# Optimization experiments

Hardware: AMD Instinct MI355X
Metric: run time of the kernel (lower is better)

The kernel has to match this reference:

```python
import jax, jax.numpy as jnp
import numpy as np

S = 1024   # query_len == key_len (self-attention)
B = 4      # batch
E = 1024   # embed_dim
H = 16     # num_heads
D = E // H # head_dim = 64
PE = 2 * S # positional table rows


def setup_inputs() -> dict:
    rng = jax.random.key(0)
    ks = jax.random.split(rng, 12)
    f = lambda k, sh, s: jax.random.normal(k, sh, dtype=jnp.float32) * s
    W = 0.02  # weight scale (xavier-ish for E=1024)
    return {
        'query': f(ks[0], (S, B, E), 1.0),
        'key': f(ks[1], (S, B, E), 1.0),
        'value': f(ks[2], (S, B, E), 1.0),
        'pe': f(ks[3], (PE, E), 1.0),
        'w_q': f(ks[4], (E, E), W),
        'w_k': f(ks[5], (E, E), W),
        'w_v': f(ks[6], (E, E), W),
        'w_k_pos': f(ks[7], (E, E), W),
        'content_bias': f(ks[8], (H, D), 0.02),
        'pos_bias': f(ks[9], (H, D), 0.02),
        'w_out': f(ks[10], (E, E), W),
        'b_out': f(ks[11], (E,), 0.02),
    }


def _rel_shift(pos):
    # pos: [B, H, Q, M] with M = 2*K - 1. Transformer-XL pad/narrow shift trick.
    Bn, h, Q, M = pos.shape
    p = jnp.pad(pos, ((0, 0), (0, 0), (0, 1), (0, 1)))          # [B,H,Q+1,M+1]
    p = p.reshape(Bn, h, (Q + 1) * (M + 1))
    p = p[:, :, M // 2: M // 2 + M * Q].reshape(Bn, h, Q, M)
    return p[..., :(M + 1) // 2]                                 # [B,H,Q,K]


def reference(query, key, value, pe, w_q, w_k, w_v, w_k_pos,
              content_bias, pos_bias, w_out, b_out):
    Q, Bn, Em = query.shape
    K = key.shape[0]
    h, d = content_bias.shape
    scaling = d ** -0.5

    # projections (nn.Linear: x @ W.T), split heads -> [B,H,len,d]
    q = (query @ w_q.T).reshape(Q, Bn, h, d).transpose(1, 2, 0, 3)
    k = (key   @ w_k.T).reshape(K, Bn, h, d).transpose(1, 2, 0, 3)
    v = (value @ w_v.T).reshape(K, Bn, h, d).transpose(1, 2, 0, 3)

    # relative position keys: centered slice of pe table, size 2K-1
    M = 2 * K - 1
    lower = pe.shape[0] // 2 - K + 1  # offset = 0
    k_pos = (pe[lower:lower + M] @ w_k_pos.T).reshape(M, h, d).transpose(1, 0, 2)  # [H,M,d]

    content = jnp.einsum('bhqd,bhkd->bhqk', q + content_bias[None, :, None, :], k)
    pos = jnp.einsum('bhqd,hmd->bhqm', q + pos_bias[None, :, None, :], k_pos)
    pos = _rel_shift(pos)  # [B,H,Q,K]

    attn = jax.nn.softmax((content + pos) * scaling, axis=-1)
    out = jnp.einsum('bhqk,bhkd->bhqd', attn, v)        # [B,H,Q,d]
    out = out.transpose(2, 0, 1, 3).reshape(Q, Bn, Em)  # [Q,B,E]
    return out @ w_out.T + b_out
```

## Files before the change

### kernel.cpp

```cpp
#include <hip/hip_runtime.h>


typedef short s16x8 __attribute__((ext_vector_type(8)));
typedef __bf16 bf16x8 __attribute__((ext_vector_type(8)));
typedef float f32x4 __attribute__((ext_vector_type(4)));
typedef unsigned int u32;

__device__ __forceinline__ float b2f(short s) {
  u32 u = ((u32)(unsigned short)s) << 16;
  return __builtin_bit_cast(float, u);
}
__device__ __forceinline__ short f2b(float f) {
  u32 u = __builtin_bit_cast(u32, f);
  u32 r = u + 0x7FFFu + ((u >> 16) & 1u);
  return (short)(r >> 16);
}

__device__ __forceinline__ f32x4 mfma_bf16(s16x8 a, s16x8 b, f32x4 c) {
  return __builtin_amdgcn_mfma_f32_16x16x32_bf16(
      __builtin_bit_cast(bf16x8, a), __builtin_bit_cast(bf16x8, b), c, 0, 0, 0);
}

__device__ __forceinline__ void glds16(void* l, const void* g) {
  __builtin_amdgcn_global_load_lds(
      (const __attribute__((address_space(1))) void*)g,
      (__attribute__((address_space(3))) void*)l, 16, 0, 0);
}

__device__ __forceinline__ int swz(int row, int unit) {
  return row * 128 + ((unit ^ (row & 7)) << 4);
}

__global__ __launch_bounds__(256) void cvt_all(
    const float* __restrict__ q, const float* __restrict__ k,
    const float* __restrict__ v, const float* __restrict__ pe,
    const float* __restrict__ wq, const float* __restrict__ wk,
    const float* __restrict__ wv, const float* __restrict__ wkp,
    const float* __restrict__ wo, short* __restrict__ dst)
{
  const int c = blockIdx.x * 256 + threadIdx.x;
  int idx = c * 8;
  const float* src;
  if      (idx < 4194304)  { src = q; }
  else if (idx < 8388608)  { src = k;   idx -= 4194304; }
  else if (idx < 12582912) { src = v;   idx -= 8388608; }
  else if (idx < 14680064) { src = pe;  idx -= 12582912; }
  else if (idx < 15728640) { src = wq;  idx -= 14680064; }
  else if (idx < 16777216) { src = wk;  idx -= 15728640; }
  else if (idx < 17825792) { src = wv;  idx -= 16777216; }
  else if (idx < 18874368) { src = wkp; idx -= 17825792; }
  else                     { src = wo;  idx -= 18874368; }
  float4 x = *(const float4*)(src + idx);
  float4 y = *(const float4*)(src + idx + 4);
  s16x8 o;
  o[0] = f2b(x.x); o[1] = f2b(x.y); o[2] = f2b(x.z); o[3] = f2b(x.w);
  o[4] = f2b(y.x); o[5] = f2b(y.y); o[6] = f2b(y.z); o[7] = f2b(y.w);
  *(s16x8*)(dst + (long)c * 8) = o;
}

__device__ __forceinline__ void gemm_core_bf16(
    const short* __restrict__ A, const short* __restrict__ W,
    short* At, short* Wt, f32x4 (&acc)[4][4], int bm, int bn)
{
  const int t = threadIdx.x;
  const int lane = t & 63, w = t >> 6;
  const int wm = w >> 1, wn = w & 1;
  const int quad = lane >> 4, lo16 = lane & 15;
  const int srow = t >> 2;
  const int skc = (t & 3) * 8;
  const int soff = t * 16;

  const short* Ag0 = A + (bm * 128 + srow) * 1024 + skc;
  const short* Wg0 = W + (bn * 128 + srow) * 1024 + skc;
  char* AtB = (char*)At;
  char* WtB = (char*)Wt;

  for (int k0 = 0; k0 < 1024; k0 += 32) {
    glds16(AtB + soff,        Ag0 + k0);
    glds16(AtB + 4096 + soff, Ag0 + 64 * 1024 + k0);
    glds16(WtB + soff,        Wg0 + k0);
    glds16(WtB + 4096 + soff, Wg0 + 64 * 1024 + k0);
    __syncthreads();
    s16x8 af[4], bfr[4];
#pragma unroll
    for (int mt = 0; mt < 4; ++mt)
      af[mt] = *(const s16x8*)(At + (wm * 64 + mt * 16 + lo16) * 32 + quad * 8);
#pragma unroll
    for (int nt = 0; nt < 4; ++nt)
      bfr[nt] = *(const s16x8*)(Wt + (wn * 64 + nt * 16 + lo16) * 32 + quad * 8);
#pragma unroll
    for (int mt = 0; mt < 4; ++mt)
#pragma unroll
      for (int nt = 0; nt < 4; ++nt)
        acc[mt][nt] = mfma_bf16(af[mt], bfr[nt], acc[mt][nt]);
    __syncthreads();
  }
}

__global__ __launch_bounds__(256) void proj_gemm(
    const short* __restrict__ qsrc, const short* __restrict__ ksrc,
    const short* __restrict__ vsrc, const short* __restrict__ pesrc,
    const short* __restrict__ wqb, const short* __restrict__ wkb,
    const short* __restrict__ wvb, const short* __restrict__ wkpb,
    short* __restrict__ qo, short* __restrict__ ko,
    short* __restrict__ vo, short* __restrict__ po)
{
  const int z = blockIdx.z;
  const short* A; const short* W; int M;
  if (z == 0)      { A = qsrc;  W = wqb;  M = 4096; }
  else if (z == 1) { A = ksrc;  W = wkb;  M = 4096; }
  else if (z == 2) { A = vsrc;  W = wvb;  M = 4096; }
  else             { A = pesrc; W = wkpb; M = 2048; }
  const int bm = blockIdx.x, bn = blockIdx.y;
  if (bm * 128 >= M) return;

  __shared__ __align__(16) short At[128 * 32];
  __shared__ __align__(16) short Wt[128 * 32];
  f32x4 acc[4][4] = {};
  gemm_core_bf16(A, W, At, Wt, acc, bm, bn);

  const int t = threadIdx.x;
  const int lane = t & 63, w = t >> 6;
  const int wm = w >> 1, wn = w & 1;
  const int quad = lane >> 4, lo16 = lane & 15;
#pragma unroll
  for (int mt = 0; mt < 4; ++mt) {
#pragma unroll
    for (int nt = 0; nt < 4; ++nt) {
#pragma unroll
      for (int r = 0; r < 4; ++r) {
        int m = bm * 128 + wm * 64 + mt * 16 + quad * 4 + r;
        int n = bn * 128 + wn * 64 + nt * 16 + lo16;
        short val = f2b(acc[mt][nt][r]);
        if (z <= 1) {
          short* o = (z == 0) ? qo : ko;
          int s = m >> 2, b = m & 3, hh = n >> 6, d = n & 63;
          o[((b * 16 + hh) * 1024 + s) * 64 + d] = val;
        } else if (z == 2) {
          int s = m >> 2, b = m & 3, hh = n >> 6, d = n & 63;
          vo[((b * 16 + hh) * 64 + d) * 1024 + s] = val;
        } else {
          int hh = n >> 6, d = n & 63;
          po[(hh * 2048 + m) * 64 + d] = val;
        }
      }
    }
  }
}

__global__ __launch_bounds__(256) void out_gemm(
    const short* __restrict__ A, const short* __restrict__ W,
    const float* __restrict__ bias, float* __restrict__ out)
{
  const int bm = blockIdx.x, bn = blockIdx.y;
  __shared__ __align__(16) short At[128 * 32];
  __shared__ __align__(16) short Wt[128 * 32];
  f32x4 acc[4][4] = {};
  gemm_core_bf16(A, W, At, Wt, acc, bm, bn);

  const int t = threadIdx.x;
  const int lane = t & 63, w = t >> 6;
  const int wm = w >> 1, wn = w & 1;
  const int quad = lane >> 4, lo16 = lane & 15;
#pragma unroll
  for (int mt = 0; mt < 4; ++mt) {
#pragma unroll
    for (int nt = 0; nt < 4; ++nt) {
#pragma unroll
      for (int r = 0; r < 4; ++r) {
        int m = bm * 128 + wm * 64 + mt * 16 + quad * 4 + r;
        int n = bn * 128 + wn * 64 + nt * 16 + lo16;
        out[m * 1024 + n] = acc[mt][nt][r] + bias[n];
      }
    }
  }
}

__global__ __launch_bounds__(256) void attn_kernel(
    const short* __restrict__ qatt, const short* __restrict__ katt,
    const short* __restrict__ vT, const short* __restrict__ kpe,
    const float* __restrict__ cbias, const float* __restrict__ pbias,
    short* __restrict__ aout)
{
  const int q0 = blockIdx.x * 64;
  const int h = blockIdx.y;
  const int b = blockIdx.z;
  const int bh = b * 16 + h;
  const int t = threadIdx.x;
  const int w = t >> 6, lane = t & 63;
  const int quad = lane >> 4, lo16 = lane & 15;

  __shared__ __align__(16) char KtB[64 * 128];
  __shared__ __align__(16) char VtB[64 * 128];
  __shared__ __align__(16) char KPB[128 * 128];
  __shared__ __align__(16) char PtB[4][16 * 128];
  char* Pt_w = PtB[w];

  s16x8 a_c[2], a_p[2];
  {
    const int qg = q0 + 16 * w + lo16;
    const short* qrow = qatt + (bh * 1024 + qg) * 64;
#pragma unroll
    for (int ds = 0; ds < 2; ++ds) {
      const int d0 = ds * 32 + quad * 8;
      s16x8 qv = *(const s16x8*)(qrow + d0);
#pragma unroll
      for (int j = 0; j < 8; ++j) {
        float qf = b2f(qv[j]);
        a_c[ds][j] = f2b(qf + cbias[h * 64 + d0 + j]);
        a_p[ds][j] = f2b(qf + pbias[h * 64 + d0 + j]);
      }
    }
  }

  f32x4 O[4] = {};
  float lrow[4] = {0.f, 0.f, 0.f, 0.f};

  const int ro = 48 - 16 * w;

  const char* kattB = (const char*)(katt + (size_t)bh * 65536);
  const char* vTB   = (const char*)(vT   + (size_t)bh * 65536);
  const char* kpeB  = (const char*)(kpe  + (size_t)h * 131072);

  for (int kt = 0; kt < 16; ++kt) {
    const int k0 = kt * 64;
    __syncthreads();
#pragma unroll
    for (int i = 0; i < 2; ++i) {
      const int o = t + 256 * i, row = o >> 3, u = (o & 7) ^ (row & 7);
      glds16(KtB + o * 16, kattB + ((k0 + row) << 7) + (u << 4));
      glds16(VtB + o * 16, vTB + (row << 11) + (k0 << 1) + (u << 4));
    }
#pragma unroll
    for (int i = 0; i < 4; ++i) {
      const int o = t + 256 * i, row = o >> 3, u = (o & 7) ^ (row & 7);
      int j = 961 + k0 - q0 + row;
      if (j > 2047) j = 2047;
      glds16(KPB + o * 16, kpeB + (j << 7) + (u << 4));
    }
    __syncthreads();

    float rot_cur[4];
    {
      f32x4 a = {0.f, 0.f, 0.f, 0.f};
      const int row = ro + lo16;
#pragma unroll
      for (int ds = 0; ds < 2; ++ds) {
        s16x8 bf = *(const s16x8*)(KPB + swz(row, ds * 4 + quad));
        a = mfma_bf16(a_p[ds], bf, a);
      }
#pragma unroll
      for (int r = 0; r < 4; ++r) {
        const int qi = quad * 4 + r;
        const int srclane = quad * 16 + ((lo16 + 15 - qi) & 15);
        rot_cur[r] = __shfl(a[r], srclane, 64);
      }
    }
#pragma unroll
    for (int nt = 0; nt < 4; ++nt) {
      f32x4 spn = {0.f, 0.f, 0.f, 0.f};
      {
        const int row = ro + (nt + 1) * 16 + lo16;
#pragma unroll
        for (int ds = 0; ds < 2; ++ds) {
          s16x8 bf = *(const s16x8*)(KPB + swz(row, ds * 4 + quad));
          spn = mfma_bf16(a_p[ds], bf, spn);
        }
      }
      f32x4 sc = {0.f, 0.f, 0.f, 0.f};
      {
        const int row = nt * 16 + lo16;
#pragma unroll
        for (int ds = 0; ds < 2; ++ds) {
          s16x8 bf = *(const s16x8*)(KtB + swz(row, ds * 4 + quad));
          sc = mfma_bf16(a_c[ds], bf, sc);
        }
      }
#pragma unroll
      for (int r = 0; r < 4; ++r) {
        const int qi = quad * 4 + r;
        const int so = lo16 + 15 - qi;
        const int srclane = quad * 16 + (so & 15);
        const float rot_next = __shfl(spn[r], srclane, 64);
        const float pos = (so >= 16) ? rot_next : rot_cur[r];
        const float p = __builtin_exp2f((sc[r] + pos) * 0.1803368801111244f);
        const short pb = f2b(p);
        lrow[r] += b2f(pb);
        const int col = nt * 16 + lo16;
        *(short*)(Pt_w + qi * 128 + (((col >> 3) ^ (qi & 7)) << 4) +
                  ((col & 7) << 1)) = pb;
        rot_cur[r] = rot_next;
      }
    }
    __builtin_amdgcn_wave_barrier();

    s16x8 ap[2];
#pragma unroll
    for (int ks = 0; ks < 2; ++ks)
      ap[ks] = *(const s16x8*)(Pt_w + swz(lo16, ks * 4 + quad));
    __builtin_amdgcn_wave_barrier();

#pragma unroll
    for (int ntd = 0; ntd < 4; ++ntd) {
#pragma unroll
      for (int ks = 0; ks < 2; ++ks) {
        s16x8 bv = *(const s16x8*)(VtB + swz(ntd * 16 + lo16, ks * 4 + quad));
        O[ntd] = mfma_bf16(ap[ks], bv, O[ntd]);
      }
    }
  }

#pragma unroll
  for (int r = 0; r < 4; ++r) {
#pragma unroll
    for (int off = 1; off < 16; off <<= 1)
      lrow[r] += __shfl_xor(lrow[r], off, 64);
    float rl = 1.f / lrow[r];
    int qg = q0 + 16 * w + quad * 4 + r;
#pragma unroll
    for (int ntd = 0; ntd < 4; ++ntd) {
      int d = ntd * 16 + lo16;
      aout[(qg * 4 + b) * 1024 + h * 64 + d] = f2b(O[ntd][r] * rl);
    }
  }
}

extern "C" void kernel_launch(void* const* d_in, const int* in_sizes, int n_in,
                              void* d_out, int out_size, void* d_ws, size_t ws_size,
                              hipStream_t stream) {
  (void)in_sizes; (void)n_in; (void)out_size; (void)ws_size;
  const float* query = (const float*)d_in[0];
  const float* key   = (const float*)d_in[1];
  const float* value = (const float*)d_in[2];
  const float* pe    = (const float*)d_in[3];
  const float* wq    = (const float*)d_in[4];
  const float* wk    = (const float*)d_in[5];
  const float* wv    = (const float*)d_in[6];
  const float* wkp   = (const float*)d_in[7];
  const float* cb    = (const float*)d_in[8];
  const float* pb    = (const float*)d_in[9];
  const float* wout  = (const float*)d_in[10];
  const float* bout  = (const float*)d_in[11];

  short* ws    = (short*)d_ws;
  short* qsrc  = ws;
  short* ksrc  = ws + 4194304;
  short* vsrc  = ws + 8388608;
  short* pesrc = ws + 12582912;
  short* wqb   = ws + 14680064;
  short* wkb   = ws + 15728640;
  short* wvb   = ws + 16777216;
  short* wkpb  = ws + 17825792;
  short* woutb = ws + 18874368;
  short* qatt  = ws + 19922944;
  short* katt  = ws + 24117248;
  short* vT    = ws + 28311552;
  short* kpe   = ws + 32505856;
  short* aout  = qsrc;

  cvt_all<<<dim3(9728), 256, 0, stream>>>(
      query, key, value, pe, wq, wk, wv, wkp, wout, ws);
  proj_gemm<<<dim3(32, 8, 4), 256, 0, stream>>>(
      qsrc, ksrc, vsrc, pesrc, wqb, wkb, wvb, wkpb, qatt, katt, vT, kpe);
  attn_kernel<<<dim3(16, 16, 4), 256, 0, stream>>>(
      qatt, katt, vT, kpe, cb, pb, aout);
  out_gemm<<<dim3(32, 8), 256, 0, stream>>>(aout, woutb, bout, (float*)d_out);
}
```

Baseline: 304.5 us.

## Double-buffer K, V and positional tiles in attention kernel with async LDS prefetch

Allocates two LDS buffers each for the K, V and positional-key tiles and issues the global-to-LDS loads for tile kt+2 while tile kt is being computed. A partial vmcnt wait plus a raw s_barrier replaces the two __syncthreads per iteration. The goal is to hide global load latency behind the MFMA and softmax work. In exchange, LDS use roughly doubles, which may cut occupancy, and the last iterations issue redundant loads of a dummy tile.

```diff
diff --git a/kernel.cpp b/kernel.cpp
--- a/kernel.cpp
+++ b/kernel.cpp
@@ -176,6 +176,26 @@
   }
 }
 
+__device__ __forceinline__ void stage_attn(
+    char* KtD, char* VtD, char* KPD,
+    const char* gK, const char* gV, const char* gP,
+    int k0, int q0, int t)
+{
+#pragma unroll
+  for (int i = 0; i < 2; ++i) {
+    const int o = t + 256 * i, row = o >> 3, u = (o & 7) ^ (row & 7);
+    glds16(KtD + o * 16, gK + ((k0 + row) << 7) + (u << 4));
+    glds16(VtD + o * 16, gV + (row << 11) + (k0 << 1) + (u << 4));
+  }
+#pragma unroll
+  for (int i = 0; i < 4; ++i) {
+    const int o = t + 256 * i, row = o >> 3, u = (o & 7) ^ (row & 7);
+    int j = 961 + k0 - q0 + row;
+    if (j > 2047) j = 2047;
+    glds16(KPD + o * 16, gP + (j << 7) + (u << 4));
+  }
+}
+
 __global__ __launch_bounds__(256) void attn_kernel(
     const short* __restrict__ qatt, const short* __restrict__ katt,
     const short* __restrict__ vT, const short* __restrict__ kpe,
@@ -190,9 +210,9 @@
   const int w = t >> 6, lane = t & 63;
   const int quad = lane >> 4, lo16 = lane & 15;
 
-  __shared__ __align__(16) char KtB[64 * 128];
-  __shared__ __align__(16) char VtB[64 * 128];
-  __shared__ __align__(16) char KPB[128 * 128];
+  __shared__ __align__(16) char KtB[2][64 * 128];
+  __shared__ __align__(16) char VtB[2][64 * 128];
+  __shared__ __align__(16) char KPB[2][128 * 128];
   __shared__ __align__(16) char PtB[4][16 * 128];
   char* Pt_w = PtB[w];
 
@@ -218,27 +238,23 @@
 
   const int ro = 48 - 16 * w;
 
-  const char* kattB = (const char*)(katt + (size_t)bh * 65536);
-  const char* vTB   = (const char*)(vT   + (size_t)bh * 65536);
-  const char* kpeB  = (const char*)(kpe  + (size_t)h * 131072);
-
+  const char* gK = (const char*)(katt + (size_t)bh * 65536);
+  const char* gV = (const char*)(vT   + (size_t)bh * 65536);
+  const char* gP = (const char*)(kpe  + (size_t)h * 131072);
+
+  stage_attn(KtB[0], VtB[0], KPB[0], gK, gV, gP, 0,  q0, t);
+  stage_attn(KtB[1], VtB[1], KPB[1], gK, gV, gP, 64, q0, t);
+
+  int cur = 0;
   for (int kt = 0; kt < 16; ++kt) {
-    const int k0 = kt * 64;
-    __syncthreads();
-#pragma unroll
-    for (int i = 0; i < 2; ++i) {
-      const int o = t + 256 * i, row = o >> 3, u = (o & 7) ^ (row & 7);
-      glds16(KtB + o * 16, kattB + ((k0 + row) << 7) + (u << 4));
-      glds16(VtB + o * 16, vTB + (row << 11) + (k0 << 1) + (u << 4));
-    }
-#pragma unroll
-    for (int i = 0; i < 4; ++i) {
-      const int o = t + 256 * i, row = o >> 3, u = (o & 7) ^ (row & 7);
-      int j = 961 + k0 - q0 + row;
-      if (j > 2047) j = 2047;
-      glds16(KPB + o * 16, kpeB + (j << 7) + (u << 4));
-    }
-    __syncthreads();
+    asm volatile("s_waitcnt vmcnt(8)" ::: "memory");
+    __builtin_amdgcn_sched_barrier(0);
+    __builtin_amdgcn_s_barrier();
+    __builtin_amdgcn_sched_barrier(0);
+
+    const char* Kc  = KtB[cur];
+    const char* Vc  = VtB[cur];
+    const char* KPc = KPB[cur];
 
     float rot_cur[4];
     {
@@ -246,7 +262,7 @@
       const int row = ro + lo16;
 #pragma unroll
       for (int ds = 0; ds < 2; ++ds) {
-        s16x8 bf = *(const s16x8*)(KPB + swz(row, ds * 4 + quad));
+        s16x8 bf = *(const s16x8*)(KPc + swz(row, ds * 4 + quad));
         a = mfma_bf16(a_p[ds], bf, a);
       }
 #pragma unroll
@@ -263,7 +279,7 @@
         const int row = ro + (nt + 1) * 16 + lo16;
 #pragma unroll
         for (int ds = 0; ds < 2; ++ds) {
-          s16x8 bf = *(const s16x8*)(KPB + swz(row, ds * 4 + quad));
+          s16x8 bf = *(const s16x8*)(KPc + swz(row, ds * 4 + quad));
           spn = mfma_bf16(a_p[ds], bf, spn);
         }
       }
@@ -272,7 +288,7 @@
         const int row = nt * 16 + lo16;
 #pragma unroll
         for (int ds = 0; ds < 2; ++ds) {
-          s16x8 bf = *(const s16x8*)(KtB + swz(row, ds * 4 + quad));
+          s16x8 bf = *(const s16x8*)(Kc + swz(row, ds * 4 + quad));
           sc = mfma_bf16(a_c[ds], bf, sc);
         }
       }
@@ -304,10 +320,18 @@
     for (int ntd = 0; ntd < 4; ++ntd) {
 #pragma unroll
       for (int ks = 0; ks < 2; ++ks) {
-        s16x8 bv = *(const s16x8*)(VtB + swz(ntd * 16 + lo16, ks * 4 + quad));
+        s16x8 bv = *(const s16x8*)(Vc + swz(ntd * 16 + lo16, ks * 4 + quad));
         O[ntd] = mfma_bf16(ap[ks], bv, O[ntd]);
       }
     }
+
+    __builtin_amdgcn_sched_barrier(0);
+    __builtin_amdgcn_s_barrier();
+    __builtin_amdgcn_sched_barrier(0);
+
+    const int kn = (kt + 2 < 16) ? (kt + 2) * 64 : 960;
+    stage_attn(KtB[cur], VtB[cur], KPB[cur], gK, gV, gP, kn, q0, t);
+    cur ^= 1;
   }
 
 #pragma unroll
```

New measurement: 292.4 us. -4.0%, faster.
